# Optimization experiments

Hardware: AMD Instinct MI355X
Metric: run time of the kernel (lower is better)

Reference implementation:

```python
import jax, jax.numpy as jnp
import numpy as np

H, D = 8, 16            # head_num, qkv_dim
E = H * D               # embedding_dim = 128
SQRT_E = float(np.sqrt(E))
LOGIT_CLIP = 10.0
MAX_DELTA = 4           # decoder_priority_bias_max_delta
TEMP = 0.8              # sampling_temperature
TOP_K = 20              # sampling_top_k


def setup_inputs() -> dict:
    key = jax.random.key(0)
    ks = jax.random.split(key, 12)
    B, P, N = 256, 200, 200
    s = 1.0 / np.sqrt(E)
    return {
        "encoded_nodes": jax.random.normal(ks[0], (B, N, E), jnp.float32),
        "encoded_first_node": jax.random.normal(ks[1], (B, P, E), jnp.float32),
        "encoded_last_node": jax.random.normal(ks[2], (B, P, E), jnp.float32),
        "ninf_mask": jnp.zeros((B, P, N), jnp.float32),
        "group_ids": jax.random.randint(ks[3], (B, N), 0, 5, jnp.int32),
        "current_min_priority": jax.random.randint(ks[4], (B, P), 0, 5, jnp.int32),
        "Wq_first": jax.random.normal(ks[5], (E, H * D), jnp.float32) * s,
        "Wq_last": jax.random.normal(ks[6], (E, H * D), jnp.float32) * s,
        "Wk": jax.random.normal(ks[7], (E, H * D), jnp.float32) * s,
        "Wv": jax.random.normal(ks[8], (E, H * D), jnp.float32) * s,
        "Wc": jax.random.normal(ks[9], (H * D, E), jnp.float32) * s,
        "bc": jax.random.normal(ks[10], (E,), jnp.float32) * 0.01,
        # learnable priority bias table: init * exp(-delta / tau)
        "bias_table": 0.2 * jnp.exp(-jnp.arange(MAX_DELTA + 1, dtype=jnp.float32)),
    }


def _heads(x):
    # [B, n, H*D] -> [B, H, n, D]
    B, n, _ = x.shape
    return x.reshape(B, n, H, D).transpose(0, 2, 1, 3)


def reference(encoded_nodes, encoded_first_node, encoded_last_node, ninf_mask,
              group_ids, current_min_priority,
              Wq_first, Wq_last, Wk, Wv, Wc, bc, bias_table):
    B, P, N = ninf_mask.shape
    # set_q1 + per-step q_last, q = q_first + q_last
    q = _heads(encoded_first_node @ Wq_first) + _heads(encoded_last_node @ Wq_last)
    k = _heads(encoded_nodes @ Wk)  # [B,H,N,D]
    v = _heads(encoded_nodes @ Wv)
    # masked multi-head attention with rank-3 ninf mask
    score = jnp.einsum('bhpd,bhnd->bhpn', q, k) / jnp.sqrt(jnp.float32(D))
    score = score + ninf_mask[:, None, :, :]
    w = jax.nn.softmax(score, axis=-1)
    out = jnp.einsum('bhpn,bhnd->bhpd', w, v)          # [B,H,P,D]
    out_concat = out.transpose(0, 2, 1, 3).reshape(B, P, H * D)
    mh = out_concat @ Wc + bc                          # multi_head_combine
    # single-head pointer attention
    sc = jnp.einsum('bpe,bne->bpn', mh, encoded_nodes)
    score_clipped = LOGIT_CLIP * jnp.tanh(sc / SQRT_E)
    # decoder priority bias (learnable table indexed by clamped delta)
    delta = jnp.clip(group_ids[:, None, :] - current_min_priority[:, :, None], 0, MAX_DELTA)
    pbias = bias_table[delta] * jnp.isfinite(ninf_mask)
    probs = jax.nn.softmax(score_clipped + pbias + ninf_mask, axis=-1)
    # sampling controls (eval): temperature then top-k filtering, renormalize
    adj = jnp.power(jnp.maximum(probs, 1e-12), 1.0 / TEMP)
    vals, idx = jax.lax.top_k(adj, TOP_K)
    bi = jnp.arange(B)[:, None, None]
    pi = jnp.arange(P)[None, :, None]
    filtered = jnp.zeros_like(adj).at[bi, pi, idx].set(vals)
    denom = jnp.maximum(filtered.sum(axis=-1, keepdims=True), 1e-12)
    return filtered / denom
```

## Files before the change

kernel.cpp:

```cpp
#include <hip/hip_runtime.h>
#include <hip/hip_bf16.h>
#include <math.h>

constexpr int B = 256, P = 200, N = 200, E = 128, H = 8, D = 16;
constexpr float INV_SQRT_D = 0.25f;
constexpr float INV_SQRT_E = 0.08838834764831845f;
constexpr float LOGIT_CLIP = 10.0f;
constexpr float INV_TEMP = 1.25f;
constexpr int TOP_K = 20;
constexpr int MAX_DELTA = 4;

__device__ __forceinline__ float dot4(float4 a, float4 b) {
    return a.x*b.x + a.y*b.y + a.z*b.z + a.w*b.w;
}

__global__ __launch_bounds__(256) void proj_kernel(
    const float* __restrict__ X1, const float* __restrict__ W1,
    const float* __restrict__ X2, const float* __restrict__ W2,
    const float* __restrict__ bias, float* __restrict__ out)
{
    __shared__ float4 xs[64][32];
    const int tid = threadIdx.x;
    const int eg = tid & 31;
    const int rg = tid >> 5;
    const int r0 = rg * 8;
    const long base = (long)blockIdx.x * 64;

    float acc[8][4];
    #pragma unroll
    for (int i = 0; i < 8; ++i)
        #pragma unroll
        for (int j = 0; j < 4; ++j) acc[i][j] = 0.f;

    for (int pass = 0; pass < 2; ++pass) {
        const float* X = pass ? X2 : X1;
        const float* W = pass ? W2 : W1;
        if (!X) break;
        if (pass) __syncthreads();
        const float4* X4 = (const float4*)X;
        for (int idx = tid; idx < 64 * 32; idx += 256) {
            int r = idx >> 5, c = idx & 31;
            xs[r][c] = X4[(base + r) * 32 + c];
        }
        __syncthreads();
        for (int c4 = 0; c4 < 32; ++c4) {
            float4 w0 = *(const float4*)&W[(c4*4+0)*128 + eg*4];
            float4 w1 = *(const float4*)&W[(c4*4+1)*128 + eg*4];
            float4 w2 = *(const float4*)&W[(c4*4+2)*128 + eg*4];
            float4 w3 = *(const float4*)&W[(c4*4+3)*128 + eg*4];
            #pragma unroll
            for (int i = 0; i < 8; ++i) {
                float4 xv = xs[r0 + i][c4];
                acc[i][0] += xv.x*w0.x + xv.y*w1.x + xv.z*w2.x + xv.w*w3.x;
                acc[i][1] += xv.x*w0.y + xv.y*w1.y + xv.z*w2.y + xv.w*w3.y;
                acc[i][2] += xv.x*w0.z + xv.y*w1.z + xv.z*w2.z + xv.w*w3.z;
                acc[i][3] += xv.x*w0.w + xv.y*w1.w + xv.z*w2.w + xv.w*w3.w;
            }
        }
    }

    float4 bv = make_float4(0.f, 0.f, 0.f, 0.f);
    if (bias) bv = *(const float4*)&bias[eg*4];
    float4* out4 = (float4*)out;
    #pragma unroll
    for (int i = 0; i < 8; ++i) {
        out4[(base + r0 + i) * 32 + eg] =
            make_float4(acc[i][0]+bv.x, acc[i][1]+bv.y, acc[i][2]+bv.z, acc[i][3]+bv.w);
    }
}

template<int TN>
__device__ __forceinline__ void attn_tile(
    int t, const float4* __restrict__ m4,
    float4 q0, float4 q1, float4 q2, float4 q3,
    const float4 (*ks)[4], const float4 (*vs)[4],
    float& m, float& l, float* o)
{
    float mvf[TN];
    #pragma unroll
    for (int j4 = 0; j4 < TN / 4; ++j4) {
        float4 mv = m4[(t >> 2) + j4];
        mvf[j4*4+0] = mv.x; mvf[j4*4+1] = mv.y;
        mvf[j4*4+2] = mv.z; mvf[j4*4+3] = mv.w;
    }
    float s[TN];
    float tmax = -INFINITY;
    #pragma unroll
    for (int j = 0; j < TN; ++j) {
        int n = t + j;
        float sc = dot4(q0, ks[n][0]) + dot4(q1, ks[n][1]) +
                   dot4(q2, ks[n][2]) + dot4(q3, ks[n][3]);
        s[j] = sc * INV_SQRT_D + mvf[j];
        tmax = fmaxf(tmax, s[j]);
    }
    float nm = fmaxf(m, tmax);
    if (nm == -INFINITY) return;
    float scale = (m == -INFINITY) ? 0.f : __expf(m - nm);
    l *= scale;
    #pragma unroll
    for (int d = 0; d < 16; ++d) o[d] *= scale;
    #pragma unroll
    for (int j = 0; j < TN; ++j) {
        int n = t + j;
        float w = __expf(s[j] - nm);
        l += w;
        float4 v0 = vs[n][0], v1 = vs[n][1], v2 = vs[n][2], v3 = vs[n][3];
        o[0]  += w*v0.x; o[1]  += w*v0.y; o[2]  += w*v0.z; o[3]  += w*v0.w;
        o[4]  += w*v1.x; o[5]  += w*v1.y; o[6]  += w*v1.z; o[7]  += w*v1.w;
        o[8]  += w*v2.x; o[9]  += w*v2.y; o[10] += w*v2.z; o[11] += w*v2.w;
        o[12] += w*v3.x; o[13] += w*v3.y; o[14] += w*v3.z; o[15] += w*v3.w;
    }
    m = nm;
}

__global__ __launch_bounds__(256) void attn_kernel(
    const float* __restrict__ q, const float* __restrict__ k,
    const float* __restrict__ v, const float* __restrict__ mask,
    float* __restrict__ out)
{
    __shared__ float4 ks[N][4];
    __shared__ float4 vs[N][4];
    const int raw = blockIdx.x;
    const int g = raw >> 6, r = raw & 63;
    const int h = r >> 3;
    const int b = g * 8 + (r & 7);
    const int tid = threadIdx.x;
    const float4* k4 = (const float4*)k;
    const float4* v4 = (const float4*)v;
    for (int idx = tid; idx < N * 4; idx += 256) {
        int n = idx >> 2, c = idx & 3;
        size_t off = (size_t)(b * N + n) * 32 + h * 4 + c;
        ks[n][c] = k4[off];
        vs[n][c] = v4[off];
    }
    __syncthreads();

    const int p = tid;
    if (p >= P) return;

    const float4* qr = (const float4*)q + (size_t)(b * P + p) * 32 + h * 4;
    float4 q0 = qr[0], q1 = qr[1], q2 = qr[2], q3 = qr[3];
    const float4* m4 = (const float4*)(mask + (size_t)(b * P + p) * N);

    float m = -INFINITY, l = 0.f;
    float o[16];
    #pragma unroll
    for (int d = 0; d < 16; ++d) o[d] = 0.f;

    for (int t = 0; t < 192; t += 16)
        attn_tile<16>(t, m4, q0, q1, q2, q3, ks, vs, m, l, o);
    attn_tile<8>(192, m4, q0, q1, q2, q3, ks, vs, m, l, o);

    float inv_l = 1.f / l;
    float4* out4 = (float4*)out;
    size_t ob = (size_t)(b * P + p) * 32 + h * 4;
    #pragma unroll
    for (int c = 0; c < 4; ++c)
        out4[ob + c] = make_float4(o[c*4]*inv_l, o[c*4+1]*inv_l,
                                   o[c*4+2]*inv_l, o[c*4+3]*inv_l);
}

__global__ __launch_bounds__(256) void pointer_kernel(
    const float* __restrict__ mh, const float* __restrict__ nodes,
    const float* __restrict__ mask, const int* __restrict__ gid,
    const int* __restrict__ cmp, const float* __restrict__ btab,
    float* __restrict__ out)
{
    __shared__ float4 ns[64][33];
    const int b = blockIdx.z;
    const int p_base = blockIdx.y * 64;
    const int n_base = blockIdx.x * 64;
    const int tid = threadIdx.x;
    const int pi = tid >> 4;
    const int ni = tid & 15;

    const float4* nodes4 = (const float4*)nodes;
    for (int idx = tid; idx < 64 * 32; idx += 256) {
        int r = idx >> 5, c = idx & 31;
        float4 val = make_float4(0.f, 0.f, 0.f, 0.f);
        if (n_base + r < N) val = nodes4[(size_t)(b * N + n_base + r) * 32 + c];
        ns[r][c] = val;
    }
    __syncthreads();

    float acc[4][4];
    #pragma unroll
    for (int i = 0; i < 4; ++i)
        #pragma unroll
        for (int j = 0; j < 4; ++j) acc[i][j] = 0.f;

    const float4* mh4 = (const float4*)mh;
    for (int c4 = 0; c4 < 32; ++c4) {
        float4 a[4];
        #pragma unroll
        for (int i = 0; i < 4; ++i) {
            int p = p_base + pi + 16 * i;
            int pr = p < P ? p : P - 1;
            a[i] = mh4[(size_t)(b * P + pr) * 32 + c4];
        }
        #pragma unroll
        for (int j = 0; j < 4; ++j) {
            float4 w = ns[ni + 16 * j][c4];
            #pragma unroll
            for (int i = 0; i < 4; ++i)
                acc[i][j] += dot4(a[i], w);
        }
    }

    float bt[MAX_DELTA + 1];
    #pragma unroll
    for (int t = 0; t <= MAX_DELTA; ++t) bt[t] = btab[t];

    #pragma unroll
    for (int i = 0; i < 4; ++i) {
        int p = p_base + pi + 16 * i;
        if (p >= P) continue;
        int cm = cmp[b * P + p];
        #pragma unroll
        for (int j = 0; j < 4; ++j) {
            int n = n_base + ni + 16 * j;
            if (n >= N) continue;
            int g = gid[b * N + n];
            int delta = g - cm;
            delta = delta < 0 ? 0 : (delta > MAX_DELTA ? MAX_DELTA : delta);
            float mv = mask[(size_t)(b * P + p) * N + n];
            float pb = isfinite(mv) ? bt[delta] : 0.f;
            float logit = LOGIT_CLIP * tanhf(acc[i][j] * INV_SQRT_E) + pb + mv;
            out[(size_t)(b * P + p) * N + n] = logit;
        }
    }
}

__global__ __launch_bounds__(256) void topk_kernel(float* __restrict__ io)
{
    const int wv = threadIdx.x >> 6, lane = threadIdx.x & 63;
    const long row = (long)blockIdx.x * 4 + wv;
    float* r = io + row * N;

    float x[4];
    unsigned u[4];
    #pragma unroll
    for (int j = 0; j < 4; ++j) {
        int n = lane + 64 * j;
        bool valid = n < N;
        x[j] = valid ? r[n] : -INFINITY;
        unsigned bb = __float_as_uint(x[j]);
        u[j] = valid ? ((bb & 0x80000000u) ? ~bb : (bb | 0x80000000u)) : 0u;
    }

    unsigned p = 0;
    for (int i = 31; i >= 0; --i) {
        unsigned c = p | (1u << i);
        int cnt = 0;
        #pragma unroll
        for (int j = 0; j < 4; ++j)
            cnt += (int)__popcll(__ballot(u[j] >= c));
        if (cnt >= TOP_K) p = c;
    }

    int cnt_gt = 0;
    #pragma unroll
    for (int j = 0; j < 4; ++j)
        cnt_gt += (int)__popcll(__ballot(u[j] > p));
    const int needed = TOP_K - cnt_gt;

    const unsigned long long lt_mask = (1ull << lane) - 1ull;
    bool sel[4];
    int eq_before = 0;
    #pragma unroll
    for (int j = 0; j < 4; ++j) {
        unsigned long long em = __ballot(u[j] == p);
        int myrank = eq_before + (int)__popcll(em & lt_mask);
        sel[j] = (u[j] > p) || ((u[j] == p) && (myrank < needed));
        eq_before += (int)__popcll(em);
    }

    unsigned tb = (p & 0x80000000u) ? (p & 0x7FFFFFFFu) : ~p;
    float Tf = __uint_as_float(tb);

    float e[4];
    float sum = 0.f;
    if (isfinite(Tf)) {
        #pragma unroll
        for (int j = 0; j < 4; ++j) {
            e[j] = sel[j] ? __expf((x[j] - Tf) * INV_TEMP) : 0.f;
            sum += e[j];
        }
    } else {
        #pragma unroll
        for (int j = 0; j < 4; ++j) {
            e[j] = sel[j] ? 1.f : 0.f;
            sum += e[j];
        }
    }
    #pragma unroll
    for (int off = 32; off > 0; off >>= 1) sum += __shfl_xor(sum, off);
    float inv = 1.f / sum;
    #pragma unroll
    for (int j = 0; j < 4; ++j) {
        int n = lane + 64 * j;
        if (n < N) r[n] = e[j] * inv;
    }
}

extern "C" void kernel_launch(void* const* d_in, const int* in_sizes, int n_in,
                              void* d_out, int out_size, void* d_ws, size_t ws_size,
                              hipStream_t stream) {
    const float* nodes = (const float*)d_in[0];
    const float* first = (const float*)d_in[1];
    const float* last  = (const float*)d_in[2];
    const float* mask  = (const float*)d_in[3];
    const int*   gid   = (const int*)d_in[4];
    const int*   cmp   = (const int*)d_in[5];
    const float* Wqf   = (const float*)d_in[6];
    const float* Wql   = (const float*)d_in[7];
    const float* Wk    = (const float*)d_in[8];
    const float* Wv    = (const float*)d_in[9];
    const float* Wc    = (const float*)d_in[10];
    const float* bc    = (const float*)d_in[11];
    const float* btab  = (const float*)d_in[12];
    float* out = (float*)d_out;

    float* ws   = (float*)d_ws;
    const size_t SLOT = (size_t)B * P * E;
    float* qb  = ws;
    float* kb  = ws + SLOT;
    float* vb  = ws + 2 * SLOT;
    float* ao  = ws + 3 * SLOT;

    const int M = B * P;

    proj_kernel<<<M / 64, 256, 0, stream>>>(first, Wqf, last, Wql, nullptr, qb);
    proj_kernel<<<M / 64, 256, 0, stream>>>(nodes, Wk, nullptr, nullptr, nullptr, kb);
    proj_kernel<<<M / 64, 256, 0, stream>>>(nodes, Wv, nullptr, nullptr, nullptr, vb);

    attn_kernel<<<B * H, 256, 0, stream>>>(qb, kb, vb, mask, ao);

    proj_kernel<<<M / 64, 256, 0, stream>>>(ao, Wc, nullptr, nullptr, bc, qb);

    dim3 pgrid((N + 63) / 64, (P + 63) / 64, B);
    pointer_kernel<<<pgrid, 256, 0, stream>>>(qb, nodes, mask, gid, cmp, btab, out);

    topk_kernel<<<(B * P) / 4, 256, 0, stream>>>(out);
}
```

Before: 678.7 us.

## Fuse K/V projections and register-block attention over four query rows per thread

Merges the separate K and V projection launches into one kernel that loads each node tile into shared memory once and produces both outputs. It also rewrites attention to use 64-thread blocks, where each thread handles four query rows and reuses each K/V shared-memory load across them. The 1/sqrt(D) scale is folded into q. This cuts LDS traffic and a launch, but raises register pressure (64 output accumulators per thread) and leaves fewer waves per block to hide latency.

```diff
diff --git a/kernel.cpp b/kernel.cpp
--- a/kernel.cpp
+++ b/kernel.cpp
@@ -69,51 +69,66 @@
     }
 }
 
-template<int TN>
-__device__ __forceinline__ void attn_tile(
-    int t, const float4* __restrict__ m4,
-    float4 q0, float4 q1, float4 q2, float4 q3,
-    const float4 (*ks)[4], const float4 (*vs)[4],
-    float& m, float& l, float* o)
+__global__ __launch_bounds__(256) void kv_proj_kernel(
+    const float* __restrict__ X, const float* __restrict__ Wk,
+    const float* __restrict__ Wv, float* __restrict__ outK,
+    float* __restrict__ outV)
 {
-    float mvf[TN];
-    #pragma unroll
-    for (int j4 = 0; j4 < TN / 4; ++j4) {
-        float4 mv = m4[(t >> 2) + j4];
-        mvf[j4*4+0] = mv.x; mvf[j4*4+1] = mv.y;
-        mvf[j4*4+2] = mv.z; mvf[j4*4+3] = mv.w;
-    }
-    float s[TN];
-    float tmax = -INFINITY;
-    #pragma unroll
-    for (int j = 0; j < TN; ++j) {
-        int n = t + j;
-        float sc = dot4(q0, ks[n][0]) + dot4(q1, ks[n][1]) +
-                   dot4(q2, ks[n][2]) + dot4(q3, ks[n][3]);
-        s[j] = sc * INV_SQRT_D + mvf[j];
-        tmax = fmaxf(tmax, s[j]);
-    }
-    float nm = fmaxf(m, tmax);
-    if (nm == -INFINITY) return;
-    float scale = (m == -INFINITY) ? 0.f : __expf(m - nm);
-    l *= scale;
-    #pragma unroll
-    for (int d = 0; d < 16; ++d) o[d] *= scale;
-    #pragma unroll
-    for (int j = 0; j < TN; ++j) {
-        int n = t + j;
-        float w = __expf(s[j] - nm);
-        l += w;
-        float4 v0 = vs[n][0], v1 = vs[n][1], v2 = vs[n][2], v3 = vs[n][3];
-        o[0]  += w*v0.x; o[1]  += w*v0.y; o[2]  += w*v0.z; o[3]  += w*v0.w;
-        o[4]  += w*v1.x; o[5]  += w*v1.y; o[6]  += w*v1.z; o[7]  += w*v1.w;
-        o[8]  += w*v2.x; o[9]  += w*v2.y; o[10] += w*v2.z; o[11] += w*v2.w;
-        o[12] += w*v3.x; o[13] += w*v3.y; o[14] += w*v3.z; o[15] += w*v3.w;
-    }
-    m = nm;
-}
-
-__global__ __launch_bounds__(256) void attn_kernel(
+    __shared__ float4 xs[64][32];
+    const int tid = threadIdx.x;
+    const int eg = tid & 31;
+    const int rg = tid >> 5;
+    const int r0 = rg * 8;
+    const long base = (long)blockIdx.x * 64;
+
+    float acck[8][4], accv[8][4];
+    #pragma unroll
+    for (int i = 0; i < 8; ++i)
+        #pragma unroll
+        for (int j = 0; j < 4; ++j) { acck[i][j] = 0.f; accv[i][j] = 0.f; }
+
+    const float4* X4 = (const float4*)X;
+    for (int idx = tid; idx < 64 * 32; idx += 256) {
+        int r = idx >> 5, c = idx & 31;
+        xs[r][c] = X4[(base + r) * 32 + c];
+    }
+    __syncthreads();
+
+    for (int c4 = 0; c4 < 32; ++c4) {
+        float4 k0 = *(const float4*)&Wk[(c4*4+0)*128 + eg*4];
+        float4 k1 = *(const float4*)&Wk[(c4*4+1)*128 + eg*4];
+        float4 k2 = *(const float4*)&Wk[(c4*4+2)*128 + eg*4];
+        float4 k3 = *(const float4*)&Wk[(c4*4+3)*128 + eg*4];
+        float4 v0 = *(const float4*)&Wv[(c4*4+0)*128 + eg*4];
+        float4 v1 = *(const float4*)&Wv[(c4*4+1)*128 + eg*4];
+        float4 v2 = *(const float4*)&Wv[(c4*4+2)*128 + eg*4];
+        float4 v3 = *(const float4*)&Wv[(c4*4+3)*128 + eg*4];
+        #pragma unroll
+        for (int i = 0; i < 8; ++i) {
+            float4 xv = xs[r0 + i][c4];
+            acck[i][0] += xv.x*k0.x + xv.y*k1.x + xv.z*k2.x + xv.w*k3.x;
+            acck[i][1] += xv.x*k0.y + xv.y*k1.y + xv.z*k2.y + xv.w*k3.y;
+            acck[i][2] += xv.x*k0.z + xv.y*k1.z + xv.z*k2.z + xv.w*k3.z;
+            acck[i][3] += xv.x*k0.w + xv.y*k1.w + xv.z*k2.w + xv.w*k3.w;
+            accv[i][0] += xv.x*v0.x + xv.y*v1.x + xv.z*v2.x + xv.w*v3.x;
+            accv[i][1] += xv.x*v0.y + xv.y*v1.y + xv.z*v2.y + xv.w*v3.y;
+            accv[i][2] += xv.x*v0.z + xv.y*v1.z + xv.z*v2.z + xv.w*v3.z;
+            accv[i][3] += xv.x*v0.w + xv.y*v1.w + xv.z*v2.w + xv.w*v3.w;
+        }
+    }
+
+    float4* outK4 = (float4*)outK;
+    float4* outV4 = (float4*)outV;
+    #pragma unroll
+    for (int i = 0; i < 8; ++i) {
+        outK4[(base + r0 + i) * 32 + eg] =
+            make_float4(acck[i][0], acck[i][1], acck[i][2], acck[i][3]);
+        outV4[(base + r0 + i) * 32 + eg] =
+            make_float4(accv[i][0], accv[i][1], accv[i][2], accv[i][3]);
+    }
+}
+
+__global__ __launch_bounds__(64, 1) void attn_kernel(
     const float* __restrict__ q, const float* __restrict__ k,
     const float* __restrict__ v, const float* __restrict__ mask,
     float* __restrict__ out)
@@ -121,13 +136,14 @@
     __shared__ float4 ks[N][4];
     __shared__ float4 vs[N][4];
     const int raw = blockIdx.x;
-    const int g = raw >> 6, r = raw & 63;
-    const int h = r >> 3;
-    const int b = g * 8 + (r & 7);
-    const int tid = threadIdx.x;
+    const int g = raw >> 6, rr6 = raw & 63;
+    const int h = rr6 >> 3;
+    const int b = g * 8 + (rr6 & 7);
+    const int t = threadIdx.x;
+
     const float4* k4 = (const float4*)k;
     const float4* v4 = (const float4*)v;
-    for (int idx = tid; idx < N * 4; idx += 256) {
+    for (int idx = t; idx < N * 4; idx += 64) {
         int n = idx >> 2, c = idx & 3;
         size_t off = (size_t)(b * N + n) * 32 + h * 4 + c;
         ks[n][c] = k4[off];
@@ -135,29 +151,109 @@
     }
     __syncthreads();
 
-    const int p = tid;
-    if (p >= P) return;
-
-    const float4* qr = (const float4*)q + (size_t)(b * P + p) * 32 + h * 4;
-    float4 q0 = qr[0], q1 = qr[1], q2 = qr[2], q3 = qr[3];
-    const float4* m4 = (const float4*)(mask + (size_t)(b * P + p) * N);
-
-    float m = -INFINITY, l = 0.f;
-    float o[16];
-    #pragma unroll
-    for (int d = 0; d < 16; ++d) o[d] = 0.f;
-
-    for (int t = 0; t < 192; t += 16)
-        attn_tile<16>(t, m4, q0, q1, q2, q3, ks, vs, m, l, o);
-    attn_tile<8>(192, m4, q0, q1, q2, q3, ks, vs, m, l, o);
-
-    float inv_l = 1.f / l;
+    float4 qv[4][4];
+    int prow[4];
+    bool act[4];
+    #pragma unroll
+    for (int r = 0; r < 4; ++r) {
+        prow[r] = t + 64 * r;
+        act[r] = prow[r] < P;
+        int pc = act[r] ? prow[r] : 0;
+        const float4* qr = (const float4*)q + (size_t)(b * P + pc) * 32 + h * 4;
+        #pragma unroll
+        for (int c = 0; c < 4; ++c) {
+            float4 x = qr[c];
+            qv[r][c] = make_float4(x.x*INV_SQRT_D, x.y*INV_SQRT_D,
+                                   x.z*INV_SQRT_D, x.w*INV_SQRT_D);
+        }
+    }
+
+    float m2[4], l[4], o[4][16];
+    #pragma unroll
+    for (int r = 0; r < 4; ++r) {
+        m2[r] = -INFINITY; l[r] = 0.f;
+        #pragma unroll
+        for (int d = 0; d < 16; ++d) o[r][d] = 0.f;
+    }
+
+    const float4* mk4 = (const float4*)mask;
+    size_t mrow[4];
+    #pragma unroll
+    for (int r = 0; r < 4; ++r)
+        mrow[r] = (size_t)(b * P + (act[r] ? prow[r] : 0)) * (N / 4);
+
+    for (int t0 = 0; t0 < N; t0 += 8) {
+        const int q4 = t0 >> 2;
+        float4 mva[4], mvb[4];
+        #pragma unroll
+        for (int r = 0; r < 4; ++r) {
+            mva[r] = mk4[mrow[r] + q4];
+            mvb[r] = mk4[mrow[r] + q4 + 1];
+        }
+        float s[4][8];
+        #pragma unroll
+        for (int j = 0; j < 8; ++j) {
+            int n = t0 + j;
+            float4 k0 = ks[n][0], k1 = ks[n][1], k2 = ks[n][2], k3 = ks[n][3];
+            #pragma unroll
+            for (int r = 0; r < 4; ++r)
+                s[r][j] = dot4(qv[r][0], k0) + dot4(qv[r][1], k1) +
+                          dot4(qv[r][2], k2) + dot4(qv[r][3], k3);
+        }
+        #pragma unroll
+        for (int r = 0; r < 4; ++r) {
+            float mvf[8] = {mva[r].x, mva[r].y, mva[r].z, mva[r].w,
+                            mvb[r].x, mvb[r].y, mvb[r].z, mvb[r].w};
+            float tmax = -INFINITY;
+            #pragma unroll
+            for (int j = 0; j < 8; ++j) {
+                s[r][j] += mvf[j];
+                tmax = fmaxf(tmax, s[r][j]);
+            }
+            float nm = fmaxf(m2[r], tmax);
+            if (nm == -INFINITY) {
+                #pragma unroll
+                for (int j = 0; j < 8; ++j) s[r][j] = 0.f;
+                continue;
+            }
+            float scale = (m2[r] == -INFINITY) ? 0.f : __expf(m2[r] - nm);
+            l[r] *= scale;
+            #pragma unroll
+            for (int d = 0; d < 16; ++d) o[r][d] *= scale;
+            #pragma unroll
+            for (int j = 0; j < 8; ++j) {
+                float w = __expf(s[r][j] - nm);
+                s[r][j] = w;
+                l[r] += w;
+            }
+            m2[r] = nm;
+        }
+        #pragma unroll
+        for (int j = 0; j < 8; ++j) {
+            int n = t0 + j;
+            float4 v0 = vs[n][0], v1 = vs[n][1], v2 = vs[n][2], v3 = vs[n][3];
+            #pragma unroll
+            for (int r = 0; r < 4; ++r) {
+                float w = s[r][j];
+                o[r][0]  += w*v0.x; o[r][1]  += w*v0.y; o[r][2]  += w*v0.z; o[r][3]  += w*v0.w;
+                o[r][4]  += w*v1.x; o[r][5]  += w*v1.y; o[r][6]  += w*v1.z; o[r][7]  += w*v1.w;
+                o[r][8]  += w*v2.x; o[r][9]  += w*v2.y; o[r][10] += w*v2.z; o[r][11] += w*v2.w;
+                o[r][12] += w*v3.x; o[r][13] += w*v3.y; o[r][14] += w*v3.z; o[r][15] += w*v3.w;
+            }
+        }
+    }
+
     float4* out4 = (float4*)out;
-    size_t ob = (size_t)(b * P + p) * 32 + h * 4;
-    #pragma unroll
-    for (int c = 0; c < 4; ++c)
-        out4[ob + c] = make_float4(o[c*4]*inv_l, o[c*4+1]*inv_l,
-                                   o[c*4+2]*inv_l, o[c*4+3]*inv_l);
+    #pragma unroll
+    for (int r = 0; r < 4; ++r) {
+        if (!act[r]) continue;
+        float inv_l = 1.f / l[r];
+        size_t ob = (size_t)(b * P + prow[r]) * 32 + h * 4;
+        #pragma unroll
+        for (int c = 0; c < 4; ++c)
+            out4[ob + c] = make_float4(o[r][c*4]*inv_l, o[r][c*4+1]*inv_l,
+                                       o[r][c*4+2]*inv_l, o[r][c*4+3]*inv_l);
+    }
 }
 
 __global__ __launch_bounds__(256) void pointer_kernel(
@@ -331,10 +427,9 @@
     const int M = B * P;
 
     proj_kernel<<<M / 64, 256, 0, stream>>>(first, Wqf, last, Wql, nullptr, qb);
-    proj_kernel<<<M / 64, 256, 0, stream>>>(nodes, Wk, nullptr, nullptr, nullptr, kb);
-    proj_kernel<<<M / 64, 256, 0, stream>>>(nodes, Wv, nullptr, nullptr, nullptr, vb);
-
-    attn_kernel<<<B * H, 256, 0, stream>>>(qb, kb, vb, mask, ao);
+    kv_proj_kernel<<<M / 64, 256, 0, stream>>>(nodes, Wk, Wv, kb, vb);
+
+    attn_kernel<<<B * H, 64, 0, stream>>>(qb, kb, vb, mask, ao);
 
     proj_kernel<<<M / 64, 256, 0, stream>>>(ao, Wc, nullptr, nullptr, bc, qb);
 
```

New measurement: 676.1 us. No clear change (-0.4%).

## Fuse K/V projections and replace online softmax with Cauchy-Schwarz bound

Applied to the files above, without the earlier changes.

K and V projections are merged into one kernel that loads each node tile once and computes both outputs. The attention kernel drops online-softmax rescaling and instead uses a fixed upper bound on the logits, the product of the query norm and the largest key norm, computed with a block reduction. This removes the per-tile max, rescale and branch work. A loose bound can underflow exp when scores sit well below it, and a non-zero mask term could push a logit above the bound.

```diff
diff --git a/kernel.cpp b/kernel.cpp
--- a/kernel.cpp
+++ b/kernel.cpp
@@ -69,48 +69,63 @@
     }
 }
 
-template<int TN>
-__device__ __forceinline__ void attn_tile(
-    int t, const float4* __restrict__ m4,
-    float4 q0, float4 q1, float4 q2, float4 q3,
-    const float4 (*ks)[4], const float4 (*vs)[4],
-    float& m, float& l, float* o)
-{
-    float mvf[TN];
-    #pragma unroll
-    for (int j4 = 0; j4 < TN / 4; ++j4) {
-        float4 mv = m4[(t >> 2) + j4];
-        mvf[j4*4+0] = mv.x; mvf[j4*4+1] = mv.y;
-        mvf[j4*4+2] = mv.z; mvf[j4*4+3] = mv.w;
-    }
-    float s[TN];
-    float tmax = -INFINITY;
-    #pragma unroll
-    for (int j = 0; j < TN; ++j) {
-        int n = t + j;
-        float sc = dot4(q0, ks[n][0]) + dot4(q1, ks[n][1]) +
-                   dot4(q2, ks[n][2]) + dot4(q3, ks[n][3]);
-        s[j] = sc * INV_SQRT_D + mvf[j];
-        tmax = fmaxf(tmax, s[j]);
-    }
-    float nm = fmaxf(m, tmax);
-    if (nm == -INFINITY) return;
-    float scale = (m == -INFINITY) ? 0.f : __expf(m - nm);
-    l *= scale;
-    #pragma unroll
-    for (int d = 0; d < 16; ++d) o[d] *= scale;
-    #pragma unroll
-    for (int j = 0; j < TN; ++j) {
-        int n = t + j;
-        float w = __expf(s[j] - nm);
-        l += w;
-        float4 v0 = vs[n][0], v1 = vs[n][1], v2 = vs[n][2], v3 = vs[n][3];
-        o[0]  += w*v0.x; o[1]  += w*v0.y; o[2]  += w*v0.z; o[3]  += w*v0.w;
-        o[4]  += w*v1.x; o[5]  += w*v1.y; o[6]  += w*v1.z; o[7]  += w*v1.w;
-        o[8]  += w*v2.x; o[9]  += w*v2.y; o[10] += w*v2.z; o[11] += w*v2.w;
-        o[12] += w*v3.x; o[13] += w*v3.y; o[14] += w*v3.z; o[15] += w*v3.w;
-    }
-    m = nm;
+__global__ __launch_bounds__(256) void kv_proj_kernel(
+    const float* __restrict__ X, const float* __restrict__ Wk,
+    const float* __restrict__ Wv, float* __restrict__ outK,
+    float* __restrict__ outV)
+{
+    __shared__ float4 xs[64][32];
+    const int tid = threadIdx.x;
+    const int eg = tid & 31;
+    const int rg = tid >> 5;
+    const int r0 = rg * 8;
+    const long base = (long)blockIdx.x * 64;
+
+    float acck[8][4], accv[8][4];
+    #pragma unroll
+    for (int i = 0; i < 8; ++i)
+        #pragma unroll
+        for (int j = 0; j < 4; ++j) { acck[i][j] = 0.f; accv[i][j] = 0.f; }
+
+    const float4* X4 = (const float4*)X;
+    for (int idx = tid; idx < 64 * 32; idx += 256) {
+        int r = idx >> 5, c = idx & 31;
+        xs[r][c] = X4[(base + r) * 32 + c];
+    }
+    __syncthreads();
+
+    for (int c4 = 0; c4 < 32; ++c4) {
+        float4 k0 = *(const float4*)&Wk[(c4*4+0)*128 + eg*4];
+        float4 k1 = *(const float4*)&Wk[(c4*4+1)*128 + eg*4];
+        float4 k2 = *(const float4*)&Wk[(c4*4+2)*128 + eg*4];
+        float4 k3 = *(const float4*)&Wk[(c4*4+3)*128 + eg*4];
+        float4 v0 = *(const float4*)&Wv[(c4*4+0)*128 + eg*4];
+        float4 v1 = *(const float4*)&Wv[(c4*4+1)*128 + eg*4];
+        float4 v2 = *(const float4*)&Wv[(c4*4+2)*128 + eg*4];
+        float4 v3 = *(const float4*)&Wv[(c4*4+3)*128 + eg*4];
+        #pragma unroll
+        for (int i = 0; i < 8; ++i) {
+            float4 xv = xs[r0 + i][c4];
+            acck[i][0] += xv.x*k0.x + xv.y*k1.x + xv.z*k2.x + xv.w*k3.x;
+            acck[i][1] += xv.x*k0.y + xv.y*k1.y + xv.z*k2.y + xv.w*k3.y;
+            acck[i][2] += xv.x*k0.z + xv.y*k1.z + xv.z*k2.z + xv.w*k3.z;
+            acck[i][3] += xv.x*k0.w + xv.y*k1.w + xv.z*k2.w + xv.w*k3.w;
+            accv[i][0] += xv.x*v0.x + xv.y*v1.x + xv.z*v2.x + xv.w*v3.x;
+            accv[i][1] += xv.x*v0.y + xv.y*v1.y + xv.z*v2.y + xv.w*v3.y;
+            accv[i][2] += xv.x*v0.z + xv.y*v1.z + xv.z*v2.z + xv.w*v3.z;
+            accv[i][3] += xv.x*v0.w + xv.y*v1.w + xv.z*v2.w + xv.w*v3.w;
+        }
+    }
+
+    float4* outK4 = (float4*)outK;
+    float4* outV4 = (float4*)outV;
+    #pragma unroll
+    for (int i = 0; i < 8; ++i) {
+        outK4[(base + r0 + i) * 32 + eg] =
+            make_float4(acck[i][0], acck[i][1], acck[i][2], acck[i][3]);
+        outV4[(base + r0 + i) * 32 + eg] =
+            make_float4(accv[i][0], accv[i][1], accv[i][2], accv[i][3]);
+    }
 }
 
 __global__ __launch_bounds__(256) void attn_kernel(
@@ -120,11 +135,13 @@
 {
     __shared__ float4 ks[N][4];
     __shared__ float4 vs[N][4];
+    __shared__ float red[4];
     const int raw = blockIdx.x;
-    const int g = raw >> 6, r = raw & 63;
-    const int h = r >> 3;
-    const int b = g * 8 + (r & 7);
+    const int g = raw >> 6, rr6 = raw & 63;
+    const int h = rr6 >> 3;
+    const int b = g * 8 + (rr6 & 7);
     const int tid = threadIdx.x;
+
     const float4* k4 = (const float4*)k;
     const float4* v4 = (const float4*)v;
     for (int idx = tid; idx < N * 4; idx += 256) {
@@ -135,21 +152,55 @@
     }
     __syncthreads();
 
+    float nrm = 0.f;
+    if (tid < N) {
+        float4 a0 = ks[tid][0], a1 = ks[tid][1], a2 = ks[tid][2], a3 = ks[tid][3];
+        nrm = dot4(a0,a0) + dot4(a1,a1) + dot4(a2,a2) + dot4(a3,a3);
+    }
+    float wm = nrm;
+    #pragma unroll
+    for (int off = 32; off > 0; off >>= 1) wm = fmaxf(wm, __shfl_xor(wm, off));
+    if ((tid & 63) == 0) red[tid >> 6] = wm;
+    __syncthreads();
+    const float kmax2 = fmaxf(fmaxf(red[0], red[1]), fmaxf(red[2], red[3]));
+
     const int p = tid;
     if (p >= P) return;
 
     const float4* qr = (const float4*)q + (size_t)(b * P + p) * 32 + h * 4;
     float4 q0 = qr[0], q1 = qr[1], q2 = qr[2], q3 = qr[3];
+    q0.x*=INV_SQRT_D; q0.y*=INV_SQRT_D; q0.z*=INV_SQRT_D; q0.w*=INV_SQRT_D;
+    q1.x*=INV_SQRT_D; q1.y*=INV_SQRT_D; q1.z*=INV_SQRT_D; q1.w*=INV_SQRT_D;
+    q2.x*=INV_SQRT_D; q2.y*=INV_SQRT_D; q2.z*=INV_SQRT_D; q2.w*=INV_SQRT_D;
+    q3.x*=INV_SQRT_D; q3.y*=INV_SQRT_D; q3.z*=INV_SQRT_D; q3.w*=INV_SQRT_D;
+    const float qn2 = dot4(q0,q0) + dot4(q1,q1) + dot4(q2,q2) + dot4(q3,q3);
+    const float M = sqrtf(qn2 * kmax2);
+
     const float4* m4 = (const float4*)(mask + (size_t)(b * P + p) * N);
 
-    float m = -INFINITY, l = 0.f;
+    float l = 0.f;
     float o[16];
     #pragma unroll
     for (int d = 0; d < 16; ++d) o[d] = 0.f;
 
-    for (int t = 0; t < 192; t += 16)
-        attn_tile<16>(t, m4, q0, q1, q2, q3, ks, vs, m, l, o);
-    attn_tile<8>(192, m4, q0, q1, q2, q3, ks, vs, m, l, o);
+    #pragma unroll 2
+    for (int n4 = 0; n4 < N / 4; ++n4) {
+        float4 mv = m4[n4];
+        float mvf[4] = {mv.x, mv.y, mv.z, mv.w};
+        #pragma unroll
+        for (int j = 0; j < 4; ++j) {
+            int n = n4 * 4 + j;
+            float s = dot4(q0, ks[n][0]) + dot4(q1, ks[n][1]) +
+                      dot4(q2, ks[n][2]) + dot4(q3, ks[n][3]);
+            float w = __expf(s + mvf[j] - M);
+            l += w;
+            float4 v0 = vs[n][0], v1 = vs[n][1], v2 = vs[n][2], v3 = vs[n][3];
+            o[0]  += w*v0.x; o[1]  += w*v0.y; o[2]  += w*v0.z; o[3]  += w*v0.w;
+            o[4]  += w*v1.x; o[5]  += w*v1.y; o[6]  += w*v1.z; o[7]  += w*v1.w;
+            o[8]  += w*v2.x; o[9]  += w*v2.y; o[10] += w*v2.z; o[11] += w*v2.w;
+            o[12] += w*v3.x; o[13] += w*v3.y; o[14] += w*v3.z; o[15] += w*v3.w;
+        }
+    }
 
     float inv_l = 1.f / l;
     float4* out4 = (float4*)out;
@@ -331,8 +382,7 @@
     const int M = B * P;
 
     proj_kernel<<<M / 64, 256, 0, stream>>>(first, Wqf, last, Wql, nullptr, qb);
-    proj_kernel<<<M / 64, 256, 0, stream>>>(nodes, Wk, nullptr, nullptr, nullptr, kb);
-    proj_kernel<<<M / 64, 256, 0, stream>>>(nodes, Wv, nullptr, nullptr, nullptr, vb);
+    kv_proj_kernel<<<M / 64, 256, 0, stream>>>(nodes, Wk, Wv, kb, vb);
 
     attn_kernel<<<B * H, 256, 0, stream>>>(qb, kb, vb, mask, ao);
 
```

After: 622.5 us. 1.09x faster.
